# Kernel tuning notes

Measured on AMD Instinct MI355X. Metric: run time of the kernel, lower is better.

Reference implementation:

```python
import jax, jax.numpy as jnp
import numpy as np

N_NODES = 40000
N_EDGES = 640000
D_IN = 128
D_OUT = 128

def setup_inputs() -> dict:
    key = jax.random.key(0)
    k1, k2, k3, k4, k5 = jax.random.split(key, 5)
    x = jax.random.normal(k1, (N_NODES, D_IN), dtype=jnp.float32)
    src = jax.random.randint(k2, (N_EDGES,), 0, N_NODES, dtype=jnp.int32)
    dst = jax.random.randint(k3, (N_EDGES,), 0, N_NODES, dtype=jnp.int32)
    W = jax.random.normal(k4, (D_OUT, D_IN), dtype=jnp.float32) * (1.0 / np.sqrt(D_IN))
    b = jax.random.normal(k5, (D_OUT,), dtype=jnp.float32) * 0.01
    return {"x": x, "src": src, "dst": dst, "W": W, "b": b}

def reference(x, src, dst, W, b):
    # message passing: each edge carries src feature; sum into dst node
    msgs = x[src]                                   # [E, D_in] gather
    h = jax.ops.segment_sum(msgs, dst, num_segments=N_NODES)  # [N, D_in]
    # linear projection (nn.Linear: h @ W.T + b)
    return h @ W.T + b
```

## Files before the change

### kernel.cpp

```cpp
#include <hip/hip_runtime.h>


#define NN 40000
#define NE 640000
#define DIM 128
#define CAP 48

#define NR 313
#define RCAP 3072
#define DIST_BLOCKS 313
#define CVX_BLOCKS 5000

typedef __attribute__((ext_vector_type(8))) short bf16x8;
typedef __attribute__((ext_vector_type(4))) float f32x4;

__device__ __forceinline__ unsigned short f2bf(float f) {
    unsigned u = __float_as_uint(f);
    unsigned r = u + 0x7FFFu + ((u >> 16) & 1u);
    return (unsigned short)(r >> 16);
}
__device__ __forceinline__ float bflo(unsigned u) { return __uint_as_float(u << 16); }
__device__ __forceinline__ float bfhi(unsigned u) { return __uint_as_float(u & 0xffff0000u); }

__global__ void zero_grc(int* __restrict__ grc) {
    int i = threadIdx.x;
    if (i < NR) grc[i] = 0;
}

__global__ __launch_bounds__(256) void prep(const float* __restrict__ x,
                                            const float* __restrict__ W,
                                            const int* __restrict__ src,
                                            const int* __restrict__ dst,
                                            int* __restrict__ grc,
                                            unsigned int* __restrict__ region,
                                            unsigned short* __restrict__ xb,
                                            unsigned short* __restrict__ Wb) {
    __shared__ int hist[NR];
    __shared__ int base[NR];
    int bid = blockIdx.x;
    int t = threadIdx.x;
    if (bid < DIST_BLOCKS) {
        for (int i = t; i < NR; i += 256) hist[i] = 0;
        __syncthreads();
        int e0 = bid * 2048;
        int dv[8], sv[8], rg[8], rk[8];
#pragma unroll
        for (int q = 0; q < 8; ++q) {
            int e = e0 + q * 256 + t;
            if (e < NE) { dv[q] = dst[e]; sv[q] = src[e]; } else dv[q] = -1;
        }
#pragma unroll
        for (int q = 0; q < 8; ++q) {
            if (dv[q] >= 0) { rg[q] = dv[q] >> 7; rk[q] = atomicAdd(&hist[rg[q]], 1); }
        }
        __syncthreads();
        for (int i = t; i < NR; i += 256) {
            int hct = hist[i];
            base[i] = hct ? atomicAdd(&grc[i], hct) : 0;
        }
        __syncthreads();
#pragma unroll
        for (int q = 0; q < 8; ++q) {
            if (dv[q] >= 0) {
                int p = base[rg[q]] + rk[q];
                if ((unsigned)p < (unsigned)RCAP)
                    region[rg[q] * RCAP + p] =
                        ((unsigned)sv[q] & 0xFFFFu) | (((unsigned)dv[q] & 127u) << 16);
            }
        }
    } else if (bid < DIST_BLOCKS + CVX_BLOCKS) {
        int i = ((bid - DIST_BLOCKS) * 256 + t) * 4;
        const float4 v = *(const float4*)(x + i);
        ushort4 o;
        o.x = f2bf(v.x); o.y = f2bf(v.y); o.z = f2bf(v.z); o.w = f2bf(v.w);
        *(ushort4*)(xb + i) = o;
    } else {
        int i = ((bid - DIST_BLOCKS - CVX_BLOCKS) * 256 + t) * 4;
        const float4 v = *(const float4*)(W + i);
        ushort4 o;
        o.x = f2bf(v.x); o.y = f2bf(v.y); o.z = f2bf(v.z); o.w = f2bf(v.w);
        *(ushort4*)(Wb + i) = o;
    }
}

__global__ __launch_bounds__(256) void build_bins(const int* __restrict__ grc,
                                                  const unsigned int* __restrict__ region,
                                                  unsigned short* __restrict__ binsg,
                                                  int* __restrict__ counts) {
    __shared__ int cnt[128];
    __shared__ unsigned short slot[128 * CAP];
    int r = blockIdx.x;
    int t = threadIdx.x;
    if (t < 128) cnt[t] = 0;
    __syncthreads();
    int n_r = grc[r];
    if (n_r > RCAP) n_r = RCAP;
    if (n_r < 0) n_r = 0;
    const unsigned int* rp = region + r * RCAP;
    for (int i = t; i < n_r; i += 256) {
        unsigned v = rp[i];
        int nd = (v >> 16) & 127;
        int c = atomicAdd(&cnt[nd], 1);
        if (c < CAP) slot[nd * CAP + c] = (unsigned short)(v & 0xFFFFu);
    }
    __syncthreads();
    if (t < 128) {
        int c = cnt[t];
        counts[r * 128 + t] = c < CAP ? c : CAP;
    }
    for (int i = t; i < 768; i += 256)
        ((uint4*)binsg)[r * 768 + i] = ((const uint4*)slot)[i];
}

#define FG_STRIDE 136

__global__ __launch_bounds__(256) void gcn_main(const unsigned short* __restrict__ xb,
                                                const int* __restrict__ counts,
                                                const unsigned short* __restrict__ binsg,
                                                const unsigned short* __restrict__ Wb,
                                                const float* __restrict__ bias,
                                                float* __restrict__ out) {
    __shared__ unsigned short hs[16 * FG_STRIDE];

    int wv = threadIdx.x >> 6;
    int lane = threadIdx.x & 63;
    int g = lane >> 4;
    int fl = lane & 15;
    int n0 = blockIdx.x * 16;

    int4 cnt4 = *(const int4*)(counts + n0 + wv * 4);

    for (int k = 0; k < 4; ++k) {
        int nd = wv * 4 + k;
        int node = n0 + nd;
        int cnt = (k == 0) ? cnt4.x : (k == 1) ? cnt4.y : (k == 2) ? cnt4.z : cnt4.w;
        if (cnt > CAP) cnt = CAP;
        if (cnt < 0) cnt = 0;
        const unsigned short* bp = binsg + node * CAP;

        float acc[8];
#pragma unroll
        for (int j = 0; j < 8; ++j) acc[j] = 0.f;

        for (int c0 = 0; c0 < cnt; c0 += 16) {
            uint4 w0 = *(const uint4*)(bp + c0);
            uint4 w1 = *(const uint4*)(bp + c0 + 8);
            uint4 v[4];
            float sc[4];
#pragma unroll
            for (int q = 0; q < 4; ++q) {
                unsigned wd = (q == 0) ? ((g < 2) ? w0.x : w0.y)
                            : (q == 1) ? ((g < 2) ? w0.z : w0.w)
                            : (q == 2) ? ((g < 2) ? w1.x : w1.y)
                                       : ((g < 2) ? w1.z : w1.w);
                int sidx = (int)((wd >> ((g & 1) * 16)) & 0xFFFFu);
                int e = c0 + q * 4 + g;
                bool ok = e < cnt;
                sc[q] = ok ? 1.f : 0.f;
                sidx = ok ? sidx : 0;
                v[q] = *(const uint4*)(xb + (size_t)sidx * DIM + fl * 8);
            }
#pragma unroll
            for (int q = 0; q < 4; ++q) {
                acc[0] = fmaf(sc[q], bflo(v[q].x), acc[0]);
                acc[1] = fmaf(sc[q], bfhi(v[q].x), acc[1]);
                acc[2] = fmaf(sc[q], bflo(v[q].y), acc[2]);
                acc[3] = fmaf(sc[q], bfhi(v[q].y), acc[3]);
                acc[4] = fmaf(sc[q], bflo(v[q].z), acc[4]);
                acc[5] = fmaf(sc[q], bfhi(v[q].z), acc[5]);
                acc[6] = fmaf(sc[q], bflo(v[q].w), acc[6]);
                acc[7] = fmaf(sc[q], bfhi(v[q].w), acc[7]);
            }
        }
#pragma unroll
        for (int j = 0; j < 8; ++j) {
            acc[j] += __shfl_xor(acc[j], 16);
            acc[j] += __shfl_xor(acc[j], 32);
        }
        if (g == 0) {
            uint4 p;
            p.x = (unsigned)f2bf(acc[0]) | ((unsigned)f2bf(acc[1]) << 16);
            p.y = (unsigned)f2bf(acc[2]) | ((unsigned)f2bf(acc[3]) << 16);
            p.z = (unsigned)f2bf(acc[4]) | ((unsigned)f2bf(acc[5]) << 16);
            p.w = (unsigned)f2bf(acc[6]) | ((unsigned)f2bf(acc[7]) << 16);
            *(uint4*)(hs + fl * FG_STRIDE + nd * 8) = p;
        }
    }
    __syncthreads();

    int m = fl;
    int quad = g;
    bf16x8 a[4];
#pragma unroll
    for (int kb = 0; kb < 4; ++kb) {
        a[kb] = *(const bf16x8*)(hs + (kb * 4 + quad) * FG_STRIDE + m * 8);
    }
#pragma unroll
    for (int t = 0; t < 2; ++t) {
        int jt = wv * 2 + t;
        f32x4 acc4 = (f32x4){0.f, 0.f, 0.f, 0.f};
        const unsigned short* wrow = Wb + (size_t)(jt * 16 + m) * DIM + quad * 8;
#pragma unroll
        for (int kb = 0; kb < 4; ++kb) {
            bf16x8 bf = *(const bf16x8*)(wrow + kb * 32);
            acc4 = __builtin_amdgcn_mfma_f32_16x16x32_bf16(a[kb], bf, acc4, 0, 0, 0);
        }
        float bj = bias[jt * 16 + m];
#pragma unroll
        for (int r = 0; r < 4; ++r) {
            out[(size_t)(n0 + quad * 4 + r) * DIM + jt * 16 + m] = acc4[r] + bj;
        }
    }
}

extern "C" void kernel_launch(void* const* d_in, const int* in_sizes, int n_in,
                              void* d_out, int out_size, void* d_ws, size_t ws_size,
                              hipStream_t stream) {
    const float* x = (const float*)d_in[0];
    const int* src = (const int*)d_in[1];
    const int* dst = (const int*)d_in[2];
    const float* W = (const float*)d_in[3];
    const float* b = (const float*)d_in[4];
    float* out = (float*)d_out;

    char* ws = (char*)d_ws;
    int* grc = (int*)ws;
    unsigned int* region = (unsigned int*)(ws + 2048);
    unsigned short* binsg = (unsigned short*)(ws + 3848192);
    int* counts = (int*)(ws + 7694336);
    unsigned short* xb = (unsigned short*)(ws + 7854592);
    unsigned short* Wb = (unsigned short*)(ws + 18094592);

    zero_grc<<<1, 512, 0, stream>>>(grc);

    prep<<<DIST_BLOCKS + CVX_BLOCKS + 16, 256, 0, stream>>>(x, W, src, dst,
                                                            grc, region, xb, Wb);

    build_bins<<<NR, 256, 0, stream>>>(grc, region, binsg, counts);

    gcn_main<<<NN / 16, 256, 0, stream>>>(xb, counts, binsg, Wb, b, out);
}
```

Measured before the change: 128.4 us.

## Fuse bin building into main kernel with 64-node regions in shared memory

Drops the separate build_bins kernel. Each gcn_main block now takes one 64-node destination region, bins that region's edges into shared memory, and then does the gather and the MFMA projection. This removes one launch and the global write/read round trip of the bins and counts. In exchange the grid shrinks to 625 blocks, each wave serially handles 16 nodes and all 8 output tiles, and shared-memory use per block grows, which may reduce parallelism and occupancy.

```diff
diff --git a/kernel.cpp b/kernel.cpp
--- a/kernel.cpp
+++ b/kernel.cpp
@@ -6,8 +6,9 @@
 #define DIM 128
 #define CAP 48
 
-#define NR 313
-#define RCAP 3072
+#define NR 625
+#define NPR 64
+#define RCAP 1536
 #define DIST_BLOCKS 313
 #define CVX_BLOCKS 5000
 
@@ -23,7 +24,7 @@
 __device__ __forceinline__ float bfhi(unsigned u) { return __uint_as_float(u & 0xffff0000u); }
 
 __global__ void zero_grc(int* __restrict__ grc) {
-    int i = threadIdx.x;
+    int i = blockIdx.x * 256 + threadIdx.x;
     if (i < NR) grc[i] = 0;
 }
 
@@ -51,7 +52,7 @@
         }
 #pragma unroll
         for (int q = 0; q < 8; ++q) {
-            if (dv[q] >= 0) { rg[q] = dv[q] >> 7; rk[q] = atomicAdd(&hist[rg[q]], 1); }
+            if (dv[q] >= 0) { rg[q] = dv[q] >> 6; rk[q] = atomicAdd(&hist[rg[q]], 1); }
         }
         __syncthreads();
         for (int i = t; i < NR; i += 256) {
@@ -65,7 +66,7 @@
                 int p = base[rg[q]] + rk[q];
                 if ((unsigned)p < (unsigned)RCAP)
                     region[rg[q] * RCAP + p] =
-                        ((unsigned)sv[q] & 0xFFFFu) | (((unsigned)dv[q] & 127u) << 16);
+                        ((unsigned)sv[q] & 0xFFFFu) | (((unsigned)dv[q] & 63u) << 16);
             }
         }
     } else if (bid < DIST_BLOCKS + CVX_BLOCKS) {
@@ -83,15 +84,26 @@
     }
 }
 
-__global__ __launch_bounds__(256) void build_bins(const int* __restrict__ grc,
-                                                  const unsigned int* __restrict__ region,
-                                                  unsigned short* __restrict__ binsg,
-                                                  int* __restrict__ counts) {
-    __shared__ int cnt[128];
-    __shared__ unsigned short slot[128 * CAP];
+#define FG_STRIDE 136
+
+__global__ __launch_bounds__(256) void gcn_main(const unsigned short* __restrict__ xb,
+                                                const int* __restrict__ grc,
+                                                const unsigned int* __restrict__ region,
+                                                const unsigned short* __restrict__ Wb,
+                                                const float* __restrict__ bias,
+                                                float* __restrict__ out) {
+    __shared__ int cnt[NPR];
+    __shared__ unsigned short slot[NPR * CAP];
+    __shared__ unsigned short hs[4 * 16 * FG_STRIDE];
+
     int r = blockIdx.x;
     int t = threadIdx.x;
-    if (t < 128) cnt[t] = 0;
+    int wv = t >> 6;
+    int lane = t & 63;
+    int g = lane >> 4;
+    int fl = lane & 15;
+
+    if (t < NPR) cnt[t] = 0;
     __syncthreads();
     int n_r = grc[r];
     if (n_r > RCAP) n_r = RCAP;
@@ -99,50 +111,23 @@
     const unsigned int* rp = region + r * RCAP;
     for (int i = t; i < n_r; i += 256) {
         unsigned v = rp[i];
-        int nd = (v >> 16) & 127;
+        int nd = (v >> 16) & 63;
         int c = atomicAdd(&cnt[nd], 1);
         if (c < CAP) slot[nd * CAP + c] = (unsigned short)(v & 0xFFFFu);
     }
     __syncthreads();
-    if (t < 128) {
-        int c = cnt[t];
-        counts[r * 128 + t] = c < CAP ? c : CAP;
-    }
-    for (int i = t; i < 768; i += 256)
-        ((uint4*)binsg)[r * 768 + i] = ((const uint4*)slot)[i];
-}
-
-#define FG_STRIDE 136
-
-__global__ __launch_bounds__(256) void gcn_main(const unsigned short* __restrict__ xb,
-                                                const int* __restrict__ counts,
-                                                const unsigned short* __restrict__ binsg,
-                                                const unsigned short* __restrict__ Wb,
-                                                const float* __restrict__ bias,
-                                                float* __restrict__ out) {
-    __shared__ unsigned short hs[16 * FG_STRIDE];
-
-    int wv = threadIdx.x >> 6;
-    int lane = threadIdx.x & 63;
-    int g = lane >> 4;
-    int fl = lane & 15;
-    int n0 = blockIdx.x * 16;
-
-    int4 cnt4 = *(const int4*)(counts + n0 + wv * 4);
-
-    for (int k = 0; k < 4; ++k) {
-        int nd = wv * 4 + k;
-        int node = n0 + nd;
-        int cnt = (k == 0) ? cnt4.x : (k == 1) ? cnt4.y : (k == 2) ? cnt4.z : cnt4.w;
-        if (cnt > CAP) cnt = CAP;
-        if (cnt < 0) cnt = 0;
-        const unsigned short* bp = binsg + node * CAP;
+
+    for (int k = 0; k < 16; ++k) {
+        int nd = wv * 16 + k;
+        int cn = cnt[nd];
+        if (cn > CAP) cn = CAP;
+        const unsigned short* bp = slot + nd * CAP;
 
         float acc[8];
 #pragma unroll
         for (int j = 0; j < 8; ++j) acc[j] = 0.f;
 
-        for (int c0 = 0; c0 < cnt; c0 += 16) {
+        for (int c0 = 0; c0 < cn; c0 += 16) {
             uint4 w0 = *(const uint4*)(bp + c0);
             uint4 w1 = *(const uint4*)(bp + c0 + 8);
             uint4 v[4];
@@ -155,7 +140,7 @@
                                        : ((g < 2) ? w1.z : w1.w);
                 int sidx = (int)((wd >> ((g & 1) * 16)) & 0xFFFFu);
                 int e = c0 + q * 4 + g;
-                bool ok = e < cnt;
+                bool ok = e < cn;
                 sc[q] = ok ? 1.f : 0.f;
                 sidx = ok ? sidx : 0;
                 v[q] = *(const uint4*)(xb + (size_t)sidx * DIM + fl * 8);
@@ -183,21 +168,21 @@
             p.y = (unsigned)f2bf(acc[2]) | ((unsigned)f2bf(acc[3]) << 16);
             p.z = (unsigned)f2bf(acc[4]) | ((unsigned)f2bf(acc[5]) << 16);
             p.w = (unsigned)f2bf(acc[6]) | ((unsigned)f2bf(acc[7]) << 16);
-            *(uint4*)(hs + fl * FG_STRIDE + nd * 8) = p;
-        }
-    }
-    __syncthreads();
+            *(uint4*)(hs + wv * 2176 + fl * FG_STRIDE + k * 8) = p;
+        }
+    }
 
     int m = fl;
     int quad = g;
+    const unsigned short* tp = hs + wv * 2176;
     bf16x8 a[4];
 #pragma unroll
     for (int kb = 0; kb < 4; ++kb) {
-        a[kb] = *(const bf16x8*)(hs + (kb * 4 + quad) * FG_STRIDE + m * 8);
-    }
-#pragma unroll
-    for (int t = 0; t < 2; ++t) {
-        int jt = wv * 2 + t;
+        a[kb] = *(const bf16x8*)(tp + (kb * 4 + quad) * FG_STRIDE + m * 8);
+    }
+    int n0 = r * 64 + wv * 16;
+#pragma unroll
+    for (int jt = 0; jt < 8; ++jt) {
         f32x4 acc4 = (f32x4){0.f, 0.f, 0.f, 0.f};
         const unsigned short* wrow = Wb + (size_t)(jt * 16 + m) * DIM + quad * 8;
 #pragma unroll
@@ -207,8 +192,8 @@
         }
         float bj = bias[jt * 16 + m];
 #pragma unroll
-        for (int r = 0; r < 4; ++r) {
-            out[(size_t)(n0 + quad * 4 + r) * DIM + jt * 16 + m] = acc4[r] + bj;
+        for (int rr = 0; rr < 4; ++rr) {
+            out[(size_t)(n0 + quad * 4 + rr) * DIM + jt * 16 + m] = acc4[rr] + bj;
         }
     }
 }
@@ -225,18 +210,14 @@
 
     char* ws = (char*)d_ws;
     int* grc = (int*)ws;
-    unsigned int* region = (unsigned int*)(ws + 2048);
-    unsigned short* binsg = (unsigned short*)(ws + 3848192);
-    int* counts = (int*)(ws + 7694336);
-    unsigned short* xb = (unsigned short*)(ws + 7854592);
-    unsigned short* Wb = (unsigned short*)(ws + 18094592);
-
-    zero_grc<<<1, 512, 0, stream>>>(grc);
+    unsigned int* region = (unsigned int*)(ws + 4096);
+    unsigned short* xb = (unsigned short*)(ws + 3844096);
+    unsigned short* Wb = (unsigned short*)(ws + 14084096);
+
+    zero_grc<<<3, 256, 0, stream>>>(grc);
 
     prep<<<DIST_BLOCKS + CVX_BLOCKS + 16, 256, 0, stream>>>(x, W, src, dst,
                                                             grc, region, xb, Wb);
 
-    build_bins<<<NR, 256, 0, stream>>>(grc, region, binsg, counts);
-
-    gcn_main<<<NN / 16, 256, 0, stream>>>(xb, counts, binsg, Wb, b, out);
-}
+    gcn_main<<<NR, 256, 0, stream>>>(xb, grc, region, Wb, b, out);
+}
```

New measurement: 128.9 us. About the same (+0.4%).
